# Optimization experiments

Hardware: AMD Instinct MI355X
Metric: run time of the kernel (lower is better)

## Reference

```python
import jax, jax.numpy as jnp
import numpy as np

EMBED_DIM = 768
NUM_HEADS = 12
HEAD_DIM = EMBED_DIM // NUM_HEADS
IMG_LEN = 196
TXT_LEN = 1852
SEQ_LEN = IMG_LEN + TXT_LEN
BATCH = 4
NEG = -1e9


def setup_inputs() -> dict:
    key = jax.random.key(0)
    ks = jax.random.split(key, 10)
    s = 1.0 / np.sqrt(EMBED_DIM)
    return {
        "x": jax.random.normal(ks[0], (BATCH, SEQ_LEN, EMBED_DIM), jnp.float32),
        "input_padding_mask": jax.random.randint(ks[1], (BATCH, TXT_LEN), 0, 2, jnp.int32),
        "Wq": jax.random.normal(ks[2], (EMBED_DIM, EMBED_DIM), jnp.float32) * s,
        "bq": jax.random.normal(ks[3], (EMBED_DIM,), jnp.float32) * 0.01,
        "Wk": jax.random.normal(ks[4], (EMBED_DIM, EMBED_DIM), jnp.float32) * s,
        "bk": jax.random.normal(ks[5], (EMBED_DIM,), jnp.float32) * 0.01,
        "Wv": jax.random.normal(ks[6], (EMBED_DIM, EMBED_DIM), jnp.float32) * s,
        "bv": jax.random.normal(ks[7], (EMBED_DIM,), jnp.float32) * 0.01,
        "Wo": jax.random.normal(ks[8], (EMBED_DIM, EMBED_DIM), jnp.float32) * s,
        "bo": jax.random.normal(ks[9], (EMBED_DIM,), jnp.float32) * 0.01,
    }


def _prefix_causal_mask():
    # tril ones, but all rows fully attend to the image prefix columns
    m = jnp.tril(jnp.ones((SEQ_LEN, SEQ_LEN), jnp.float32))
    m = m.at[:, :IMG_LEN].set(1.0)
    return m


def reference(x, input_padding_mask, Wq, bq, Wk, bk, Wv, bv, Wo, bo):
    B, S, E = x.shape
    H, D = NUM_HEADS, HEAD_DIM
    # torch nn.Linear: y = x @ W.T + b, weight shape [out, in]
    q = (x @ Wq.T + bq).reshape(B, S, H, D).transpose(0, 2, 1, 3)  # [B,H,S,D]
    k = (x @ Wk.T + bk).reshape(B, S, H, D).transpose(0, 2, 1, 3)
    v = (x @ Wv.T + bv).reshape(B, S, H, D).transpose(0, 2, 1, 3)

    sims = jnp.einsum("bhqd,bhkd->bhqk", q, k) / jnp.sqrt(jnp.float32(D))
    mask = _prefix_causal_mask()[None, None]  # [1,1,S,S]
    sims = jnp.where(mask == 0, NEG, sims)

    # padding mask over key positions (image prefix always valid)
    full_pad = jnp.concatenate(
        [jnp.ones((B, IMG_LEN), input_padding_mask.dtype), input_padding_mask], axis=1
    )  # [B,S]
    sims = jnp.where(full_pad[:, None, None, :] == 0, NEG, sims)

    attn = jax.nn.softmax(sims, axis=-1)
    out = jnp.einsum("bhqk,bhkd->bhqd", attn, v)
    out = out.transpose(0, 2, 1, 3).reshape(B, S, E)
    return out @ Wo.T + bo
```

## Files before the change

kernel.cpp:

```cpp
#include <hip/hip_runtime.h>

#define B_ 4
#define S_ 2048
#define E_ 768
#define H_ 12
#define D_ 64
#define IMG_ 196
#define TXT_ 1852
#define NEG_ (-1e9f)

typedef __bf16 bf16x8 __attribute__((ext_vector_type(8)));
typedef float f32x4 __attribute__((ext_vector_type(4)));
typedef float f32x16 __attribute__((ext_vector_type(16)));

__device__ __forceinline__ unsigned short f2b(float f) {
    __bf16 h = (__bf16)f;
    return __builtin_bit_cast(unsigned short, h);
}
__device__ __forceinline__ unsigned int pack2(float lo, float hi) {
    return (unsigned int)f2b(lo) | ((unsigned int)f2b(hi) << 16);
}
__device__ __forceinline__ void gload16(const unsigned short* g, unsigned short* l) {
    __builtin_amdgcn_global_load_lds(
        (const __attribute__((address_space(1))) unsigned int*)g,
        (__attribute__((address_space(3))) unsigned int*)l, 16, 0, 0);
}


__global__ __launch_bounds__(256) void cvt_kernel(const float* __restrict__ src,
                                                  unsigned short* __restrict__ dst,
                                                  int n4) {
    int i = blockIdx.x * 256 + threadIdx.x;
    if (i < n4) {
        float4 f = reinterpret_cast<const float4*>(src)[i];
        ushort4 u;
        u.x = f2b(f.x); u.y = f2b(f.y); u.z = f2b(f.z); u.w = f2b(f.w);
        reinterpret_cast<ushort4*>(dst)[i] = u;
    }
}

__global__ __launch_bounds__(256) void cvtw_kernel(
    const float* __restrict__ w0, const float* __restrict__ w1,
    const float* __restrict__ w2, const float* __restrict__ w3,
    unsigned short* __restrict__ d0, unsigned short* __restrict__ d1,
    unsigned short* __restrict__ d2, unsigned short* __restrict__ d3,
    int n4) {
    int i = blockIdx.x * 256 + threadIdx.x;
    if (i >= n4) return;
    int which = blockIdx.y;
    const float* src = (which == 0) ? w0 : (which == 1) ? w1 : (which == 2) ? w2 : w3;
    unsigned short* dst = (which == 0) ? d0 : (which == 1) ? d1 : (which == 2) ? d2 : d3;
    float4 f = reinterpret_cast<const float4*>(src)[i];
    ushort4 u;
    u.x = f2b(f.x); u.y = f2b(f.y); u.z = f2b(f.z); u.w = f2b(f.w);
    reinterpret_cast<ushort4*>(dst)[i] = u;
}

__global__ __launch_bounds__(256) void padneg_kernel(const int* __restrict__ pad,
                                                     float* __restrict__ padneg) {
    int i = blockIdx.x * 256 + threadIdx.x;
    if (i < B_ * S_) {
        int b = i >> 11, s = i & 2047;
        float v = 0.f;
        if (s >= IMG_) v = pad[b * TXT_ + (s - IMG_)] ? 0.f : NEG_;
        padneg[i] = v;
    }
}

__global__ __launch_bounds__(256) void qkv_gemm(
    const unsigned short* __restrict__ xb,
    const unsigned short* __restrict__ wqb,
    const unsigned short* __restrict__ wkb,
    const unsigned short* __restrict__ wvb,
    const float* __restrict__ bq, const float* __restrict__ bk,
    const float* __restrict__ bv,
    unsigned short* __restrict__ qfb, unsigned short* __restrict__ kfb,
    unsigned short* __restrict__ vfb)
{
    __shared__ __align__(16) unsigned short As[128 * 64];
    __shared__ __align__(16) unsigned short Bs[128 * 64];
    const int m0 = blockIdx.x * 128;
    const int n0 = blockIdx.y * 128;
    const int which = n0 / E_;
    const int ncol0 = n0 % E_;
    const unsigned short* W = (which == 0) ? wqb : ((which == 1) ? wkb : wvb);
    const int t = threadIdx.x;
    const int lane = t & 63, wid = t >> 6;
    const int wr = wid >> 1, wc = wid & 1;
    const int c = lane & 15, g = lane >> 4;
    const int srow = lane >> 3;
    const int sslot = (lane & 7) ^ srow;

    f32x4 acc[4][4];
#pragma unroll
    for (int i = 0; i < 4; ++i)
#pragma unroll
        for (int j = 0; j < 4; ++j) acc[i][j] = (f32x4){0.f, 0.f, 0.f, 0.f};

    for (int k0 = 0; k0 < E_; k0 += 64) {
        __syncthreads();
#pragma unroll
        for (int j = 0; j < 8; ++j) {
            int chunk = wid * 8 + j;
            int isB = chunk >> 4;
            int ch = chunk & 15;
            int row = ch * 8 + srow;
            const unsigned short* src =
                (isB ? W + (size_t)(ncol0 + row) * E_
                     : xb + (size_t)(m0 + row) * E_) + k0 + sslot * 8;
            unsigned short* dst = (isB ? Bs : As) + ch * 512;
            gload16(src, dst);
        }
        __syncthreads();

        bf16x8 af[2][4], bfv[2][4];
#pragma unroll
        for (int kk = 0; kk < 2; ++kk) {
#pragma unroll
            for (int fr = 0; fr < 4; ++fr) {
                int row = wr * 64 + fr * 16 + c;
                af[kk][fr] = *reinterpret_cast<const bf16x8*>(
                    &As[row * 64 + (((kk * 4 + g) ^ (row & 7)) * 8)]);
            }
#pragma unroll
            for (int fc = 0; fc < 4; ++fc) {
                int row = wc * 64 + fc * 16 + c;
                bfv[kk][fc] = *reinterpret_cast<const bf16x8*>(
                    &Bs[row * 64 + (((kk * 4 + g) ^ (row & 7)) * 8)]);
            }
        }
#pragma unroll
        for (int kk = 0; kk < 2; ++kk)
#pragma unroll
            for (int fr = 0; fr < 4; ++fr)
#pragma unroll
                for (int fc = 0; fc < 4; ++fc)
                    acc[fr][fc] = __builtin_amdgcn_mfma_f32_16x16x32_bf16(
                        af[kk][fr], bfv[kk][fc], acc[fr][fc], 0, 0, 0);
    }

    const float* bias_ptr = (which == 0) ? bq : ((which == 1) ? bk : bv);
    if (which != 2) {
        unsigned short* dstbuf = (which == 0) ? qfb : kfb;
#pragma unroll
        for (int fc = 0; fc < 4; ++fc) {
            int e = ncol0 + wc * 64 + fc * 16 + c;
            float bias = bias_ptr[e];
            int hd = e >> 6, d = e & 63;
            int dc = d >> 4, hf = (d >> 3) & 1, e8 = d & 7;
#pragma unroll
            for (int fr = 0; fr < 4; ++fr) {
#pragma unroll
                for (int r = 0; r < 4; ++r) {
                    int m = m0 + wr * 64 + fr * 16 + g * 4 + r;
                    int b = m >> 11, s = m & 2047;
                    int bh = b * H_ + hd, t32 = s >> 5, sl = s & 31;
                    size_t off = ((((size_t)bh * 64 + t32) * 4 + dc) * 64
                                  + hf * 32 + sl) * 8 + e8;
                    dstbuf[off] = f2b(acc[fr][fc][r] + bias);
                }
            }
        }
    } else {
#pragma unroll
        for (int fc = 0; fc < 4; ++fc) {
            int e = ncol0 + wc * 64 + fc * 16 + c;
            float bias = bias_ptr[e];
            int hd = e >> 6, d = e & 63;
            int vh = d >> 5, dl = d & 31;
#pragma unroll
            for (int fr = 0; fr < 4; ++fr) {
                int m = m0 + wr * 64 + fr * 16 + g * 4;
                int b = m >> 11, s = m & 2047;
                int bh = b * H_ + hd, t32 = s >> 5, ks = s & 31;
                int mm = ks >> 4, hb = (ks >> 3) & 1, e8 = ks & 7;
                size_t off = (((((size_t)bh * 64 + t32) * 2 + mm) * 2 + vh) * 64
                              + hb * 32 + dl) * 8 + e8;
                uint2 pk;
                pk.x = pack2(acc[fr][fc][0] + bias, acc[fr][fc][1] + bias);
                pk.y = pack2(acc[fr][fc][2] + bias, acc[fr][fc][3] + bias);
                *reinterpret_cast<uint2*>(&vfb[off]) = pk;
            }
        }
    }
}

__global__ __launch_bounds__(256) void attn_kernel(
    const unsigned short* __restrict__ qF,
    const unsigned short* __restrict__ kF,
    const unsigned short* __restrict__ vF,
    const float* __restrict__ padneg,
    unsigned short* __restrict__ ob)
{
    __shared__ float exch[3][34 * 64];
    const int flat = blockIdx.x;
    const int xcd = flat & 7, idx = flat >> 3;
    const int bh = xcd * 6 + (idx >> 6);
    const int qt = idx & 63;
    const int b = bh / H_, hh = bh % H_;
    const int t = threadIdx.x;
    const int lane = t & 63, w = t >> 6;
    const int h = lane >> 5, ql = lane & 31;
    const int qbase = qt * 32;
    const int q = qbase + ql;
    const float* pn = padneg + b * S_;

    bf16x8 qf[4];
    {
        const unsigned short* qp = qF + ((size_t)(bh * 64 + qt) * 4) * 512 + lane * 8;
#pragma unroll
        for (int dc = 0; dc < 4; ++dc)
            qf[dc] = *reinterpret_cast<const bf16x8*>(qp + dc * 512);
    }

    f32x16 oa0, oa1;
#pragma unroll
    for (int r = 0; r < 16; ++r) { oa0[r] = 0.f; oa1[r] = 0.f; }
    float mr = -3.0e38f, lr = 0.f;

    int kmax = qbase + 32; if (kmax < IMG_) kmax = IMG_;
    const int nt = (kmax + 31) >> 5;
    const int cchunk = (nt + 3) >> 2;
    const int t0w = w * cchunk;
    const int t1w = min(nt, t0w + cchunk);
    const bool hasC = (t1w == nt) && (t0w < t1w);
    const int preEnd = hasC ? (t1w - 1) : t1w;

    const unsigned short* kbase = kF + ((size_t)bh * 64 * 4) * 512 + lane * 8;
    const unsigned short* vbase = vF + ((size_t)bh * 64 * 4) * 512 + lane * 8;

    auto pvstep = [&](const f32x16& p, int tile) {
        unsigned int pka0 = pack2(p[0], p[1]),   pkb0 = pack2(p[2], p[3]);
        unsigned int pka1 = pack2(p[4], p[5]),   pkb1 = pack2(p[6], p[7]);
        unsigned int pka2 = pack2(p[8], p[9]),   pkb2 = pack2(p[10], p[11]);
        unsigned int pka3 = pack2(p[12], p[13]), pkb3 = pack2(p[14], p[15]);
        const unsigned short* vp = vbase + (size_t)tile * 2048;
#pragma unroll
        for (int m = 0; m < 2; ++m) {
            unsigned int keep0 = h ? (m ? pka3 : pka1) : (m ? pka2 : pka0);
            unsigned int keep1 = h ? (m ? pkb3 : pkb1) : (m ? pkb2 : pkb0);
            unsigned int send0 = h ? (m ? pka2 : pka0) : (m ? pka3 : pka1);
            unsigned int send1 = h ? (m ? pkb2 : pkb0) : (m ? pkb3 : pkb1);
            unsigned int x0 = (unsigned int)__shfl_xor((int)send0, 32, 64);
            unsigned int x1 = (unsigned int)__shfl_xor((int)send1, 32, 64);
            uint4 fr;
            fr.x = h ? x0 : keep0;
            fr.y = h ? x1 : keep1;
            fr.z = h ? keep0 : x0;
            fr.w = h ? keep1 : x1;
            bf16x8 pb = __builtin_bit_cast(bf16x8, fr);
            bf16x8 vf0 = *reinterpret_cast<const bf16x8*>(vp + (m * 2 + 0) * 512);
            bf16x8 vf1 = *reinterpret_cast<const bf16x8*>(vp + (m * 2 + 1) * 512);
            oa0 = __builtin_amdgcn_mfma_f32_32x32x16_bf16(vf0, pb, oa0, 0, 0, 0);
            oa1 = __builtin_amdgcn_mfma_f32_32x32x16_bf16(vf1, pb, oa1, 0, 0, 0);
        }
    };

    auto loadpna = [&](float* pna, int k0) {
        *reinterpret_cast<float4*>(&pna[0])  = *reinterpret_cast<const float4*>(&pn[k0 + 0  + 4 * h]);
        *reinterpret_cast<float4*>(&pna[4])  = *reinterpret_cast<const float4*>(&pn[k0 + 8  + 4 * h]);
        *reinterpret_cast<float4*>(&pna[8])  = *reinterpret_cast<const float4*>(&pn[k0 + 16 + 4 * h]);
        *reinterpret_cast<float4*>(&pna[12]) = *reinterpret_cast<const float4*>(&pn[k0 + 24 + 4 * h]);
    };

    int kt = t0w;
    for (; kt + 2 <= preEnd; kt += 2) {
        const unsigned short* kpa = kbase + (size_t)kt * 2048;
        bf16x8 ka[4], kb4[4];
#pragma unroll
        for (int dc = 0; dc < 4; ++dc) {
            ka[dc]  = *reinterpret_cast<const bf16x8*>(kpa + dc * 512);
            kb4[dc] = *reinterpret_cast<const bf16x8*>(kpa + 2048 + dc * 512);
        }
        f32x16 sa, sb;
#pragma unroll
        for (int r = 0; r < 16; ++r) { sa[r] = 0.f; sb[r] = 0.f; }
#pragma unroll
        for (int dc = 0; dc < 4; ++dc) {
            sa = __builtin_amdgcn_mfma_f32_32x32x16_bf16(ka[dc],  qf[dc], sa, 0, 0, 0);
            sb = __builtin_amdgcn_mfma_f32_32x32x16_bf16(kb4[dc], qf[dc], sb, 0, 0, 0);
        }
        float pna[16], pnb[16];
        loadpna(pna, kt * 32);
        loadpna(pnb, kt * 32 + 32);
#pragma unroll
        for (int r = 0; r < 16; ++r) {
            sa[r] = fmaf(sa[r], 0.125f, pna[r]);
            sb[r] = fmaf(sb[r], 0.125f, pnb[r]);
        }
        float tm = fmaxf(sa[0], sb[0]);
#pragma unroll
        for (int r = 1; r < 16; ++r) tm = fmaxf(tm, fmaxf(sa[r], sb[r]));
        tm = fmaxf(tm, __shfl_xor(tm, 32, 64));
        if (!__all(tm - mr <= 8.f)) {
            float mnew = fmaxf(mr, tm);
            float alpha = __expf(mr - mnew);
            mr = mnew; lr *= alpha;
#pragma unroll
            for (int r = 0; r < 16; ++r) { oa0[r] *= alpha; oa1[r] *= alpha; }
        }
#pragma unroll
        for (int r = 0; r < 16; ++r) {
            sa[r] = __expf(sa[r] - mr);
            sb[r] = __expf(sb[r] - mr);
        }
        float ss = 0.f;
#pragma unroll
        for (int r = 0; r < 16; ++r) ss += sa[r] + sb[r];
        ss += __shfl_xor(ss, 32, 64);
        lr += ss;
        pvstep(sa, kt);
        pvstep(sb, kt + 1);
    }

#pragma unroll 1
    for (int pass = (kt < preEnd) ? 0 : 1; pass < (hasC ? 2 : 1); ++pass) {
        const int tile = pass ? (nt - 1) : kt;
        const bool causal = (pass == 1);
        const unsigned short* kp = kbase + (size_t)tile * 2048;
        bf16x8 kf4[4];
#pragma unroll
        for (int dc = 0; dc < 4; ++dc)
            kf4[dc] = *reinterpret_cast<const bf16x8*>(kp + dc * 512);
        f32x16 s;
#pragma unroll
        for (int r = 0; r < 16; ++r) s[r] = 0.f;
#pragma unroll
        for (int dc = 0; dc < 4; ++dc)
            s = __builtin_amdgcn_mfma_f32_32x32x16_bf16(kf4[dc], qf[dc], s, 0, 0, 0);
        const int k0 = tile * 32;
        float pna[16];
        loadpna(pna, k0);
#pragma unroll
        for (int r = 0; r < 16; ++r) s[r] = fmaf(s[r], 0.125f, pna[r]);
        if (causal) {
#pragma unroll
            for (int r = 0; r < 16; ++r) {
                int key = k0 + (r & 3) + 8 * (r >> 2) + 4 * h;
                if (!((key <= q) || (key < IMG_))) s[r] = NEG_;
            }
        }
        float tm = s[0];
#pragma unroll
        for (int r = 1; r < 16; ++r) tm = fmaxf(tm, s[r]);
        tm = fmaxf(tm, __shfl_xor(tm, 32, 64));
        if (!__all(tm - mr <= 8.f)) {
            float mnew = fmaxf(mr, tm);
            float alpha = __expf(mr - mnew);
            mr = mnew; lr *= alpha;
#pragma unroll
            for (int r = 0; r < 16; ++r) { oa0[r] *= alpha; oa1[r] *= alpha; }
        }
#pragma unroll
        for (int r = 0; r < 16; ++r) s[r] = __expf(s[r] - mr);
        float ss = 0.f;
#pragma unroll
        for (int r = 0; r < 16; ++r) ss += s[r];
        ss += __shfl_xor(ss, 32, 64);
        lr += ss;
        pvstep(s, tile);
    }

    if (w > 0) {
        float* X = exch[w - 1];
#pragma unroll
        for (int r = 0; r < 16; ++r) {
            X[r * 64 + lane] = oa0[r];
            X[(16 + r) * 64 + lane] = oa1[r];
        }
        X[32 * 64 + lane] = mr;
        X[33 * 64 + lane] = lr;
    }
    __syncthreads();
    if (w > 0) return;

    float mAll = mr;
#pragma unroll
    for (int i = 0; i < 3; ++i) mAll = fmaxf(mAll, exch[i][32 * 64 + lane]);
    float w0 = __expf(mr - mAll);
    float L = lr * w0;
#pragma unroll
    for (int r = 0; r < 16; ++r) { oa0[r] *= w0; oa1[r] *= w0; }
#pragma unroll
    for (int i = 0; i < 3; ++i) {
        float wi = __expf(exch[i][32 * 64 + lane] - mAll);
        L = fmaf(exch[i][33 * 64 + lane], wi, L);
#pragma unroll
        for (int r = 0; r < 16; ++r) {
            oa0[r] = fmaf(exch[i][r * 64 + lane], wi, oa0[r]);
            oa1[r] = fmaf(exch[i][(16 + r) * 64 + lane], wi, oa1[r]);
        }
    }

    float inv = 1.f / L;
    unsigned short* orow = ob + ((size_t)(b * S_ + q)) * E_ + hh * D_;
#pragma unroll
    for (int gg = 0; gg < 4; ++gg) {
        int d0 = gg * 8 + 4 * h;
        uint2 s0, s1;
        s0.x = pack2(oa0[4 * gg] * inv, oa0[4 * gg + 1] * inv);
        s0.y = pack2(oa0[4 * gg + 2] * inv, oa0[4 * gg + 3] * inv);
        s1.x = pack2(oa1[4 * gg] * inv, oa1[4 * gg + 1] * inv);
        s1.y = pack2(oa1[4 * gg + 2] * inv, oa1[4 * gg + 3] * inv);
        *reinterpret_cast<uint2*>(orow + d0) = s0;
        *reinterpret_cast<uint2*>(orow + 32 + d0) = s1;
    }
}

__global__ __launch_bounds__(256) void oproj_gemm(
    const unsigned short* __restrict__ ab,
    const unsigned short* __restrict__ wob,
    const float* __restrict__ bo,
    float* __restrict__ out)
{
    __shared__ __align__(16) unsigned short As[128 * 64];
    __shared__ __align__(16) unsigned short Bs[128 * 64];
    const int m0 = blockIdx.x * 128;
    const int n0 = blockIdx.y * 128;
    const int t = threadIdx.x;
    const int lane = t & 63, wid = t >> 6;
    const int wr = wid >> 1, wc = wid & 1;
    const int c = lane & 15, g = lane >> 4;
    const int srow = lane >> 3;
    const int sslot = (lane & 7) ^ srow;

    f32x4 acc[4][4];
#pragma unroll
    for (int i = 0; i < 4; ++i)
#pragma unroll
        for (int j = 0; j < 4; ++j) acc[i][j] = (f32x4){0.f, 0.f, 0.f, 0.f};

    for (int k0 = 0; k0 < E_; k0 += 64) {
        __syncthreads();
#pragma unroll
        for (int j = 0; j < 8; ++j) {
            int chunk = wid * 8 + j;
            int isB = chunk >> 4;
            int ch = chunk & 15;
            int row = ch * 8 + srow;
            const unsigned short* src =
                (isB ? wob + (size_t)(n0 + row) * E_
                     : ab + (size_t)(m0 + row) * E_) + k0 + sslot * 8;
            unsigned short* dst = (isB ? Bs : As) + ch * 512;
            gload16(src, dst);
        }
        __syncthreads();

        bf16x8 af[2][4], bfv[2][4];
#pragma unroll
        for (int kk = 0; kk < 2; ++kk) {
#pragma unroll
            for (int fr = 0; fr < 4; ++fr) {
                int row = wr * 64 + fr * 16 + c;
                af[kk][fr] = *reinterpret_cast<const bf16x8*>(
                    &As[row * 64 + (((kk * 4 + g) ^ (row & 7)) * 8)]);
            }
#pragma unroll
            for (int fc = 0; fc < 4; ++fc) {
                int row = wc * 64 + fc * 16 + c;
                bfv[kk][fc] = *reinterpret_cast<const bf16x8*>(
                    &Bs[row * 64 + (((kk * 4 + g) ^ (row & 7)) * 8)]);
            }
        }
#pragma unroll
        for (int kk = 0; kk < 2; ++kk)
#pragma unroll
            for (int fr = 0; fr < 4; ++fr)
#pragma unroll
                for (int fc = 0; fc < 4; ++fc)
                    acc[fr][fc] = __builtin_amdgcn_mfma_f32_16x16x32_bf16(
                        af[kk][fr], bfv[kk][fc], acc[fr][fc], 0, 0, 0);
    }

#pragma unroll
    for (int fc = 0; fc < 4; ++fc) {
        int n = n0 + wc * 64 + fc * 16 + c;
        float bias = bo[n];
#pragma unroll
        for (int fr = 0; fr < 4; ++fr)
#pragma unroll
            for (int r = 0; r < 4; ++r) {
                int m = m0 + wr * 64 + fr * 16 + g * 4 + r;
                out[(size_t)m * E_ + n] = acc[fr][fc][r] + bias;
            }
    }
}

extern "C" void kernel_launch(void* const* d_in, const int* in_sizes, int n_in,
                              void* d_out, int out_size, void* d_ws, size_t ws_size,
                              hipStream_t stream) {
    const float* x  = (const float*)d_in[0];
    const int* pad  = (const int*)d_in[1];
    const float* Wq = (const float*)d_in[2];
    const float* bq = (const float*)d_in[3];
    const float* Wk = (const float*)d_in[4];
    const float* bk = (const float*)d_in[5];
    const float* Wv = (const float*)d_in[6];
    const float* bv = (const float*)d_in[7];
    const float* Wo = (const float*)d_in[8];
    const float* bo = (const float*)d_in[9];
    float* out = (float*)d_out;

    const size_t NX = (size_t)B_ * S_ * E_;
    const size_t NW = (size_t)E_ * E_;
    unsigned short* ws = (unsigned short*)d_ws;
    unsigned short* xb  = ws;
    unsigned short* wqb = xb + NX;
    unsigned short* wkb = wqb + NW;
    unsigned short* wvb = wkb + NW;
    unsigned short* wob = wvb + NW;
    unsigned short* qfb = wob + NW;
    unsigned short* kfb = qfb + NX;
    unsigned short* vfb = kfb + NX;
    unsigned short* obuf = vfb + NX;
    float* padneg = (float*)(obuf + NX);

    cvt_kernel<<<(int)(NX / 4 / 256), 256, 0, stream>>>(x, xb, (int)(NX / 4));
    cvtw_kernel<<<dim3((int)(NW / 4 / 256), 4), 256, 0, stream>>>(
        Wq, Wk, Wv, Wo, wqb, wkb, wvb, wob, (int)(NW / 4));
    padneg_kernel<<<(B_ * S_) / 256, 256, 0, stream>>>(pad, padneg);

    qkv_gemm<<<dim3(64, 18), 256, 0, stream>>>(xb, wqb, wkb, wvb, bq, bk, bv,
                                               qfb, kfb, vfb);
    attn_kernel<<<dim3(3072), 256, 0, stream>>>(qfb, kfb, vfb, padneg, obuf);
    oproj_gemm<<<dim3(64, 6), 256, 0, stream>>>(obuf, wob, bo, out);
}
```

Measured before the change: 160.9 us.

## Software-pipeline K loads in attention and fold softmax scale into Q for exp2

The attention main loop becomes one per-tile STEP that double-buffers K fragments, prefetching the next tile while the current QK MFMAs run, and issues V loads early. The causal tile is handled inside the same loop instead of a separate pass. The Q projection epilogue now multiplies by scale*log2(e), so softmax can use native exp2 with no per-element multiply; the rescale threshold is converted to match. It also adds a launch-bounds occupancy hint and switches to 32-bit offsets, at the cost of higher register pressure from the prefetch buffers.

```diff
diff --git a/kernel.cpp b/kernel.cpp
--- a/kernel.cpp
+++ b/kernel.cpp
@@ -8,6 +8,9 @@
 #define IMG_ 196
 #define TXT_ 1852
 #define NEG_ (-1e9f)
+#define QSCALE_ 0.18033688f
+#define THR2_ 11.5451f
+#define EXP2_(x) __builtin_amdgcn_exp2f(x)
 
 typedef __bf16 bf16x8 __attribute__((ext_vector_type(8)));
 typedef float f32x4 __attribute__((ext_vector_type(4)));
@@ -142,6 +145,7 @@
     const float* bias_ptr = (which == 0) ? bq : ((which == 1) ? bk : bv);
     if (which != 2) {
         unsigned short* dstbuf = (which == 0) ? qfb : kfb;
+        const float oscale = (which == 0) ? QSCALE_ : 1.0f;
 #pragma unroll
         for (int fc = 0; fc < 4; ++fc) {
             int e = ncol0 + wc * 64 + fc * 16 + c;
@@ -157,7 +161,7 @@
                     int bh = b * H_ + hd, t32 = s >> 5, sl = s & 31;
                     size_t off = ((((size_t)bh * 64 + t32) * 4 + dc) * 64
                                   + hf * 32 + sl) * 8 + e8;
-                    dstbuf[off] = f2b(acc[fr][fc][r] + bias);
+                    dstbuf[off] = f2b((acc[fr][fc][r] + bias) * oscale);
                 }
             }
         }
@@ -185,7 +189,7 @@
     }
 }
 
-__global__ __launch_bounds__(256) void attn_kernel(
+__global__ __launch_bounds__(256, 4) void attn_kernel(
     const unsigned short* __restrict__ qF,
     const unsigned short* __restrict__ kF,
     const unsigned short* __restrict__ vF,
@@ -205,12 +209,15 @@
     const int q = qbase + ql;
     const float* pn = padneg + b * S_;
 
+    const int bhoff = bh * 131072;
+    const int laneoff = lane * 8;
+
     bf16x8 qf[4];
     {
-        const unsigned short* qp = qF + ((size_t)(bh * 64 + qt) * 4) * 512 + lane * 8;
+        int off = bhoff + qt * 2048 + laneoff;
 #pragma unroll
         for (int dc = 0; dc < 4; ++dc)
-            qf[dc] = *reinterpret_cast<const bf16x8*>(qp + dc * 512);
+            qf[dc] = *reinterpret_cast<const bf16x8*>(qF + off + dc * 512);
     }
 
     f32x16 oa0, oa1;
@@ -220,21 +227,67 @@
 
     int kmax = qbase + 32; if (kmax < IMG_) kmax = IMG_;
     const int nt = (kmax + 31) >> 5;
+    const int ntm1 = nt - 1;
     const int cchunk = (nt + 3) >> 2;
     const int t0w = w * cchunk;
     const int t1w = min(nt, t0w + cchunk);
-    const bool hasC = (t1w == nt) && (t0w < t1w);
-    const int preEnd = hasC ? (t1w - 1) : t1w;
-
-    const unsigned short* kbase = kF + ((size_t)bh * 64 * 4) * 512 + lane * 8;
-    const unsigned short* vbase = vF + ((size_t)bh * 64 * 4) * 512 + lane * 8;
-
-    auto pvstep = [&](const f32x16& p, int tile) {
-        unsigned int pka0 = pack2(p[0], p[1]),   pkb0 = pack2(p[2], p[3]);
-        unsigned int pka1 = pack2(p[4], p[5]),   pkb1 = pack2(p[6], p[7]);
-        unsigned int pka2 = pack2(p[8], p[9]),   pkb2 = pack2(p[10], p[11]);
-        unsigned int pka3 = pack2(p[12], p[13]), pkb3 = pack2(p[14], p[15]);
-        const unsigned short* vp = vbase + (size_t)tile * 2048;
+
+    int koff = bhoff + t0w * 2048 + laneoff;
+    int pnoff = t0w * 32;
+
+    auto STEP = [&](bf16x8 (&kc)[4], bf16x8 (&kn)[4], int kt) {
+        f32x16 s;
+#pragma unroll
+        for (int r = 0; r < 16; ++r) s[r] = 0.f;
+#pragma unroll
+        for (int dc = 0; dc < 4; ++dc)
+            s = __builtin_amdgcn_mfma_f32_32x32x16_bf16(kc[dc], qf[dc], s, 0, 0, 0);
+        if (kt + 1 < t1w) {
+#pragma unroll
+            for (int dc = 0; dc < 4; ++dc)
+                kn[dc] = *reinterpret_cast<const bf16x8*>(kF + (koff + 2048) + dc * 512);
+        }
+        bf16x8 vf[4];
+#pragma unroll
+        for (int j = 0; j < 4; ++j)
+            vf[j] = *reinterpret_cast<const bf16x8*>(vF + koff + j * 512);
+
+#pragma unroll
+        for (int gg = 0; gg < 4; ++gg) {
+            float4 p4 = *reinterpret_cast<const float4*>(pn + pnoff + gg * 8 + 4 * h);
+            s[4 * gg + 0] += p4.x; s[4 * gg + 1] += p4.y;
+            s[4 * gg + 2] += p4.z; s[4 * gg + 3] += p4.w;
+        }
+        if (kt == ntm1) {
+#pragma unroll
+            for (int r = 0; r < 16; ++r) {
+                int key = pnoff + (r & 3) + 8 * (r >> 2) + 4 * h;
+                if (!((key <= q) || (key < IMG_))) s[r] = NEG_;
+            }
+        }
+        float tm = s[0];
+#pragma unroll
+        for (int r = 1; r < 16; ++r) tm = fmaxf(tm, s[r]);
+        tm = fmaxf(tm, __shfl_xor(tm, 32, 64));
+        if (!__all(tm - mr <= THR2_)) {
+            float mnew = fmaxf(mr, tm);
+            float alpha = EXP2_(mr - mnew);
+            mr = mnew; lr *= alpha;
+#pragma unroll
+            for (int r = 0; r < 16; ++r) { oa0[r] *= alpha; oa1[r] *= alpha; }
+        }
+#pragma unroll
+        for (int r = 0; r < 16; ++r) s[r] = EXP2_(s[r] - mr);
+        float ss = 0.f;
+#pragma unroll
+        for (int r = 0; r < 16; ++r) ss += s[r];
+        ss += __shfl_xor(ss, 32, 64);
+        lr += ss;
+
+        unsigned int pka0 = pack2(s[0], s[1]),   pkb0 = pack2(s[2], s[3]);
+        unsigned int pka1 = pack2(s[4], s[5]),   pkb1 = pack2(s[6], s[7]);
+        unsigned int pka2 = pack2(s[8], s[9]),   pkb2 = pack2(s[10], s[11]);
+        unsigned int pka3 = pack2(s[12], s[13]), pkb3 = pack2(s[14], s[15]);
 #pragma unroll
         for (int m = 0; m < 2; ++m) {
             unsigned int keep0 = h ? (m ? pka3 : pka1) : (m ? pka2 : pka0);
@@ -249,117 +302,21 @@
             fr.z = h ? keep0 : x0;
             fr.w = h ? keep1 : x1;
             bf16x8 pb = __builtin_bit_cast(bf16x8, fr);
-            bf16x8 vf0 = *reinterpret_cast<const bf16x8*>(vp + (m * 2 + 0) * 512);
-            bf16x8 vf1 = *reinterpret_cast<const bf16x8*>(vp + (m * 2 + 1) * 512);
-            oa0 = __builtin_amdgcn_mfma_f32_32x32x16_bf16(vf0, pb, oa0, 0, 0, 0);
-            oa1 = __builtin_amdgcn_mfma_f32_32x32x16_bf16(vf1, pb, oa1, 0, 0, 0);
-        }
+            oa0 = __builtin_amdgcn_mfma_f32_32x32x16_bf16(vf[2 * m + 0], pb, oa0, 0, 0, 0);
+            oa1 = __builtin_amdgcn_mfma_f32_32x32x16_bf16(vf[2 * m + 1], pb, oa1, 0, 0, 0);
+        }
+        koff += 2048; pnoff += 32;
     };
 
-    auto loadpna = [&](float* pna, int k0) {
-        *reinterpret_cast<float4*>(&pna[0])  = *reinterpret_cast<const float4*>(&pn[k0 + 0  + 4 * h]);
-        *reinterpret_cast<float4*>(&pna[4])  = *reinterpret_cast<const float4*>(&pn[k0 + 8  + 4 * h]);
-        *reinterpret_cast<float4*>(&pna[8])  = *reinterpret_cast<const float4*>(&pn[k0 + 16 + 4 * h]);
-        *reinterpret_cast<float4*>(&pna[12]) = *reinterpret_cast<const float4*>(&pn[k0 + 24 + 4 * h]);
-    };
-
+    bf16x8 kA[4], kB[4];
+    if (t0w < t1w) {
+#pragma unroll
+        for (int dc = 0; dc < 4; ++dc)
+            kA[dc] = *reinterpret_cast<const bf16x8*>(kF + koff + dc * 512);
+    }
     int kt = t0w;
-    for (; kt + 2 <= preEnd; kt += 2) {
-        const unsigned short* kpa = kbase + (size_t)kt * 2048;
-        bf16x8 ka[4], kb4[4];
-#pragma unroll
-        for (int dc = 0; dc < 4; ++dc) {
-            ka[dc]  = *reinterpret_cast<const bf16x8*>(kpa + dc * 512);
-            kb4[dc] = *reinterpret_cast<const bf16x8*>(kpa + 2048 + dc * 512);
-        }
-        f32x16 sa, sb;
-#pragma unroll
-        for (int r = 0; r < 16; ++r) { sa[r] = 0.f; sb[r] = 0.f; }
-#pragma unroll
-        for (int dc = 0; dc < 4; ++dc) {
-            sa = __builtin_amdgcn_mfma_f32_32x32x16_bf16(ka[dc],  qf[dc], sa, 0, 0, 0);
-            sb = __builtin_amdgcn_mfma_f32_32x32x16_bf16(kb4[dc], qf[dc], sb, 0, 0, 0);
-        }
-        float pna[16], pnb[16];
-        loadpna(pna, kt * 32);
-        loadpna(pnb, kt * 32 + 32);
-#pragma unroll
-        for (int r = 0; r < 16; ++r) {
-            sa[r] = fmaf(sa[r], 0.125f, pna[r]);
-            sb[r] = fmaf(sb[r], 0.125f, pnb[r]);
-        }
-        float tm = fmaxf(sa[0], sb[0]);
-#pragma unroll
-        for (int r = 1; r < 16; ++r) tm = fmaxf(tm, fmaxf(sa[r], sb[r]));
-        tm = fmaxf(tm, __shfl_xor(tm, 32, 64));
-        if (!__all(tm - mr <= 8.f)) {
-            float mnew = fmaxf(mr, tm);
-            float alpha = __expf(mr - mnew);
-            mr = mnew; lr *= alpha;
-#pragma unroll
-            for (int r = 0; r < 16; ++r) { oa0[r] *= alpha; oa1[r] *= alpha; }
-        }
-#pragma unroll
-        for (int r = 0; r < 16; ++r) {
-            sa[r] = __expf(sa[r] - mr);
-            sb[r] = __expf(sb[r] - mr);
-        }
-        float ss = 0.f;
-#pragma unroll
-        for (int r = 0; r < 16; ++r) ss += sa[r] + sb[r];
-        ss += __shfl_xor(ss, 32, 64);
-        lr += ss;
-        pvstep(sa, kt);
-        pvstep(sb, kt + 1);
-    }
-
-#pragma unroll 1
-    for (int pass = (kt < preEnd) ? 0 : 1; pass < (hasC ? 2 : 1); ++pass) {
-        const int tile = pass ? (nt - 1) : kt;
-        const bool causal = (pass == 1);
-        const unsigned short* kp = kbase + (size_t)tile * 2048;
-        bf16x8 kf4[4];
-#pragma unroll
-        for (int dc = 0; dc < 4; ++dc)
-            kf4[dc] = *reinterpret_cast<const bf16x8*>(kp + dc * 512);
-        f32x16 s;
-#pragma unroll
-        for (int r = 0; r < 16; ++r) s[r] = 0.f;
-#pragma unroll
-        for (int dc = 0; dc < 4; ++dc)
-            s = __builtin_amdgcn_mfma_f32_32x32x16_bf16(kf4[dc], qf[dc], s, 0, 0, 0);
-        const int k0 = tile * 32;
-        float pna[16];
-        loadpna(pna, k0);
-#pragma unroll
-        for (int r = 0; r < 16; ++r) s[r] = fmaf(s[r], 0.125f, pna[r]);
-        if (causal) {
-#pragma unroll
-            for (int r = 0; r < 16; ++r) {
-                int key = k0 + (r & 3) + 8 * (r >> 2) + 4 * h;
-                if (!((key <= q) || (key < IMG_))) s[r] = NEG_;
-            }
-        }
-        float tm = s[0];
-#pragma unroll
-        for (int r = 1; r < 16; ++r) tm = fmaxf(tm, s[r]);
-        tm = fmaxf(tm, __shfl_xor(tm, 32, 64));
-        if (!__all(tm - mr <= 8.f)) {
-            float mnew = fmaxf(mr, tm);
-            float alpha = __expf(mr - mnew);
-            mr = mnew; lr *= alpha;
-#pragma unroll
-            for (int r = 0; r < 16; ++r) { oa0[r] *= alpha; oa1[r] *= alpha; }
-        }
-#pragma unroll
-        for (int r = 0; r < 16; ++r) s[r] = __expf(s[r] - mr);
-        float ss = 0.f;
-#pragma unroll
-        for (int r = 0; r < 16; ++r) ss += s[r];
-        ss += __shfl_xor(ss, 32, 64);
-        lr += ss;
-        pvstep(s, tile);
-    }
+    for (; kt + 2 <= t1w; kt += 2) { STEP(kA, kB, kt); STEP(kB, kA, kt + 1); }
+    if (kt < t1w) STEP(kA, kB, kt);
 
     if (w > 0) {
         float* X = exch[w - 1];
@@ -377,13 +334,13 @@
     float mAll = mr;
 #pragma unroll
     for (int i = 0; i < 3; ++i) mAll = fmaxf(mAll, exch[i][32 * 64 + lane]);
-    float w0 = __expf(mr - mAll);
+    float w0 = EXP2_(mr - mAll);
     float L = lr * w0;
 #pragma unroll
     for (int r = 0; r < 16; ++r) { oa0[r] *= w0; oa1[r] *= w0; }
 #pragma unroll
     for (int i = 0; i < 3; ++i) {
-        float wi = __expf(exch[i][32 * 64 + lane] - mAll);
+        float wi = EXP2_(exch[i][32 * 64 + lane] - mAll);
         L = fmaf(exch[i][33 * 64 + lane], wi, L);
 #pragma unroll
         for (int r = 0; r < 16; ++r) {
```

New measurement: 174.0 us. 1.08x slower.

## Fold softmax scale and log2e into Q, use exp2, prefetch V, reverse tiles

Applied to the files above, without the earlier changes.

The Q projection epilogue now multiplies by 0.125*log2(e), so the attention loop drops its per-score scale FMA and uses the hardware exp2 in place of __expf. The rescale threshold is adjusted to the base-2 domain. V fragments are loaded right after the QK MFMAs rather than inside the PV step, which hides their latency behind the softmax math. Query tiles are issued in reverse order so the longer causal rows start first. The cost is that Q is rounded to bf16 after scaling, which changes rounding slightly.

```diff
diff --git a/kernel.cpp b/kernel.cpp
--- a/kernel.cpp
+++ b/kernel.cpp
@@ -8,6 +8,9 @@
 #define IMG_ 196
 #define TXT_ 1852
 #define NEG_ (-1e9f)
+#define QSCALE_ 0.18033688f
+#define THR2_ 11.5451f
+#define EXP2_(x) __builtin_amdgcn_exp2f(x)
 
 typedef __bf16 bf16x8 __attribute__((ext_vector_type(8)));
 typedef float f32x4 __attribute__((ext_vector_type(4)));
@@ -142,6 +145,7 @@
     const float* bias_ptr = (which == 0) ? bq : ((which == 1) ? bk : bv);
     if (which != 2) {
         unsigned short* dstbuf = (which == 0) ? qfb : kfb;
+        const float oscale = (which == 0) ? QSCALE_ : 1.0f;
 #pragma unroll
         for (int fc = 0; fc < 4; ++fc) {
             int e = ncol0 + wc * 64 + fc * 16 + c;
@@ -157,7 +161,7 @@
                     int bh = b * H_ + hd, t32 = s >> 5, sl = s & 31;
                     size_t off = ((((size_t)bh * 64 + t32) * 4 + dc) * 64
                                   + hf * 32 + sl) * 8 + e8;
-                    dstbuf[off] = f2b(acc[fr][fc][r] + bias);
+                    dstbuf[off] = f2b((acc[fr][fc][r] + bias) * oscale);
                 }
             }
         }
@@ -196,7 +200,7 @@
     const int flat = blockIdx.x;
     const int xcd = flat & 7, idx = flat >> 3;
     const int bh = xcd * 6 + (idx >> 6);
-    const int qt = idx & 63;
+    const int qt = 63 - (idx & 63);
     const int b = bh / H_, hh = bh % H_;
     const int t = threadIdx.x;
     const int lane = t & 63, w = t >> 6;
@@ -229,12 +233,11 @@
     const unsigned short* kbase = kF + ((size_t)bh * 64 * 4) * 512 + lane * 8;
     const unsigned short* vbase = vF + ((size_t)bh * 64 * 4) * 512 + lane * 8;
 
-    auto pvstep = [&](const f32x16& p, int tile) {
+    auto pvstep = [&](const f32x16& p, const bf16x8 (&vf)[4]) {
         unsigned int pka0 = pack2(p[0], p[1]),   pkb0 = pack2(p[2], p[3]);
         unsigned int pka1 = pack2(p[4], p[5]),   pkb1 = pack2(p[6], p[7]);
         unsigned int pka2 = pack2(p[8], p[9]),   pkb2 = pack2(p[10], p[11]);
         unsigned int pka3 = pack2(p[12], p[13]), pkb3 = pack2(p[14], p[15]);
-        const unsigned short* vp = vbase + (size_t)tile * 2048;
 #pragma unroll
         for (int m = 0; m < 2; ++m) {
             unsigned int keep0 = h ? (m ? pka3 : pka1) : (m ? pka2 : pka0);
@@ -249,10 +252,8 @@
             fr.z = h ? keep0 : x0;
             fr.w = h ? keep1 : x1;
             bf16x8 pb = __builtin_bit_cast(bf16x8, fr);
-            bf16x8 vf0 = *reinterpret_cast<const bf16x8*>(vp + (m * 2 + 0) * 512);
-            bf16x8 vf1 = *reinterpret_cast<const bf16x8*>(vp + (m * 2 + 1) * 512);
-            oa0 = __builtin_amdgcn_mfma_f32_32x32x16_bf16(vf0, pb, oa0, 0, 0, 0);
-            oa1 = __builtin_amdgcn_mfma_f32_32x32x16_bf16(vf1, pb, oa1, 0, 0, 0);
+            oa0 = __builtin_amdgcn_mfma_f32_32x32x16_bf16(vf[2 * m + 0], pb, oa0, 0, 0, 0);
+            oa1 = __builtin_amdgcn_mfma_f32_32x32x16_bf16(vf[2 * m + 1], pb, oa1, 0, 0, 0);
         }
     };
 
@@ -280,37 +281,46 @@
             sa = __builtin_amdgcn_mfma_f32_32x32x16_bf16(ka[dc],  qf[dc], sa, 0, 0, 0);
             sb = __builtin_amdgcn_mfma_f32_32x32x16_bf16(kb4[dc], qf[dc], sb, 0, 0, 0);
         }
+        bf16x8 va[4], vb[4];
+        {
+            const unsigned short* vpa = vbase + (size_t)kt * 2048;
+#pragma unroll
+            for (int j = 0; j < 4; ++j) {
+                va[j] = *reinterpret_cast<const bf16x8*>(vpa + j * 512);
+                vb[j] = *reinterpret_cast<const bf16x8*>(vpa + 2048 + j * 512);
+            }
+        }
         float pna[16], pnb[16];
         loadpna(pna, kt * 32);
         loadpna(pnb, kt * 32 + 32);
 #pragma unroll
         for (int r = 0; r < 16; ++r) {
-            sa[r] = fmaf(sa[r], 0.125f, pna[r]);
-            sb[r] = fmaf(sb[r], 0.125f, pnb[r]);
+            sa[r] += pna[r];
+            sb[r] += pnb[r];
         }
         float tm = fmaxf(sa[0], sb[0]);
 #pragma unroll
         for (int r = 1; r < 16; ++r) tm = fmaxf(tm, fmaxf(sa[r], sb[r]));
         tm = fmaxf(tm, __shfl_xor(tm, 32, 64));
-        if (!__all(tm - mr <= 8.f)) {
+        if (!__all(tm - mr <= THR2_)) {
             float mnew = fmaxf(mr, tm);
-            float alpha = __expf(mr - mnew);
+            float alpha = EXP2_(mr - mnew);
             mr = mnew; lr *= alpha;
 #pragma unroll
             for (int r = 0; r < 16; ++r) { oa0[r] *= alpha; oa1[r] *= alpha; }
         }
 #pragma unroll
         for (int r = 0; r < 16; ++r) {
-            sa[r] = __expf(sa[r] - mr);
-            sb[r] = __expf(sb[r] - mr);
+            sa[r] = EXP2_(sa[r] - mr);
+            sb[r] = EXP2_(sb[r] - mr);
         }
         float ss = 0.f;
 #pragma unroll
         for (int r = 0; r < 16; ++r) ss += sa[r] + sb[r];
         ss += __shfl_xor(ss, 32, 64);
         lr += ss;
-        pvstep(sa, kt);
-        pvstep(sb, kt + 1);
+        pvstep(sa, va);
+        pvstep(sb, vb);
     }
 
 #pragma unroll 1
@@ -328,11 +338,18 @@
 #pragma unroll
         for (int dc = 0; dc < 4; ++dc)
             s = __builtin_amdgcn_mfma_f32_32x32x16_bf16(kf4[dc], qf[dc], s, 0, 0, 0);
+        bf16x8 vt[4];
+        {
+            const unsigned short* vp = vbase + (size_t)tile * 2048;
+#pragma unroll
+            for (int j = 0; j < 4; ++j)
+                vt[j] = *reinterpret_cast<const bf16x8*>(vp + j * 512);
+        }
         const int k0 = tile * 32;
         float pna[16];
         loadpna(pna, k0);
 #pragma unroll
-        for (int r = 0; r < 16; ++r) s[r] = fmaf(s[r], 0.125f, pna[r]);
+        for (int r = 0; r < 16; ++r) s[r] += pna[r];
         if (causal) {
 #pragma unroll
             for (int r = 0; r < 16; ++r) {
@@ -344,21 +361,21 @@
 #pragma unroll
         for (int r = 1; r < 16; ++r) tm = fmaxf(tm, s[r]);
         tm = fmaxf(tm, __shfl_xor(tm, 32, 64));
-        if (!__all(tm - mr <= 8.f)) {
+        if (!__all(tm - mr <= THR2_)) {
             float mnew = fmaxf(mr, tm);
-            float alpha = __expf(mr - mnew);
+            float alpha = EXP2_(mr - mnew);
             mr = mnew; lr *= alpha;
 #pragma unroll
             for (int r = 0; r < 16; ++r) { oa0[r] *= alpha; oa1[r] *= alpha; }
         }
 #pragma unroll
-        for (int r = 0; r < 16; ++r) s[r] = __expf(s[r] - mr);
+        for (int r = 0; r < 16; ++r) s[r] = EXP2_(s[r] - mr);
         float ss = 0.f;
 #pragma unroll
         for (int r = 0; r < 16; ++r) ss += s[r];
         ss += __shfl_xor(ss, 32, 64);
         lr += ss;
-        pvstep(s, tile);
+        pvstep(s, vt);
     }
 
     if (w > 0) {
@@ -377,13 +394,13 @@
     float mAll = mr;
 #pragma unroll
     for (int i = 0; i < 3; ++i) mAll = fmaxf(mAll, exch[i][32 * 64 + lane]);
-    float w0 = __expf(mr - mAll);
+    float w0 = EXP2_(mr - mAll);
     float L = lr * w0;
 #pragma unroll
     for (int r = 0; r < 16; ++r) { oa0[r] *= w0; oa1[r] *= w0; }
 #pragma unroll
     for (int i = 0; i < 3; ++i) {
-        float wi = __expf(exch[i][32 * 64 + lane] - mAll);
+        float wi = EXP2_(exch[i][32 * 64 + lane] - mAll);
         L = fmaf(exch[i][33 * 64 + lane], wi, L);
 #pragma unroll
         for (int r = 0; r < 16; ++r) {
```

Measured after the change: 151.7 us. 5.7% less time.
